# Kernel tuning notes

Hardware: AMD Instinct MI355X
Metric: run time of the kernel (lower is better)

The kernel has to match this reference:

```python
import jax, jax.numpy as jnp
import numpy as np

THETA = 10000.0
NUM_HEADS = 16


def _rope(x, positions):
    # x: [B, H, S, Dk] (fp32), positions: [B, S] int
    d_k = x.shape[-1]
    k = jnp.arange(0, d_k, 2, dtype=jnp.float32)
    freqs = THETA ** (-k / d_k)                      # [Dk/2]
    angles = positions[..., None].astype(jnp.float32) * freqs  # [B, S, Dk/2]
    cos = jnp.cos(angles)[:, None, :, :]             # [B, 1, S, Dk/2]
    sin = jnp.sin(angles)[:, None, :, :]
    xr = x.reshape(*x.shape[:-1], d_k // 2, 2)
    x_even, x_odd = xr[..., 0], xr[..., 1]
    rot_even = x_even * cos - x_odd * sin
    rot_odd = x_even * sin + x_odd * cos
    out = jnp.stack([rot_even, rot_odd], axis=-1)
    return out.reshape(x.shape)


def setup_inputs() -> dict:
    key = jax.random.key(0)
    ks = jax.random.split(key, 6)
    B, S, D = 2, 2048, 1024
    std = (2.0 / (D + D)) ** 0.5
    x = jax.random.normal(ks[0], (B, S, D), dtype=jnp.float32)
    Wq = jax.random.normal(ks[1], (D, D), dtype=jnp.float32) * std
    Wk = jax.random.normal(ks[2], (D, D), dtype=jnp.float32) * std
    Wv = jax.random.normal(ks[3], (D, D), dtype=jnp.float32) * std
    Wo = jax.random.normal(ks[4], (D, D), dtype=jnp.float32) * std
    token_positions = jnp.broadcast_to(jnp.arange(S, dtype=jnp.int32), (B, S))
    return {"x": x, "Wq": Wq, "Wk": Wk, "Wv": Wv, "Wo": Wo,
            "token_positions": token_positions}


def reference(x, Wq, Wk, Wv, Wo, token_positions):
    B, S, D = x.shape
    H = NUM_HEADS
    Dk = D // H
    # QKV projections (no bias): y = x @ W.T
    def proj(W):
        return (x @ W.T).reshape(B, S, H, Dk).transpose(0, 2, 1, 3)  # [B,H,S,Dk]
    Q, K, V = proj(Wq), proj(Wk), proj(Wv)
    Q = _rope(Q, token_positions)
    K = _rope(K, token_positions)
    scale = 1.0 / jnp.sqrt(jnp.float32(Dk))
    scores = jnp.einsum('bhqd,bhkd->bhqk', Q, K) * scale  # [B,H,S,S]
    causal = jnp.tril(jnp.ones((S, S), dtype=bool))
    scores = jnp.where(causal, scores, -jnp.inf)
    attn = jax.nn.softmax(scores.astype(jnp.float32), axis=-1)
    out = jnp.einsum('bhqk,bhkd->bhqd', attn, V)          # [B,H,S,Dk]
    out = out.transpose(0, 2, 1, 3).reshape(B, S, D)
    return out @ Wo.T
```

## Files before the change

### kernel.cpp

```cpp
#include <hip/hip_runtime.h>
#include <math.h>

#define D_MODEL 1024
#define NHEADS 16
#define DK 64
#define SEQ 2048
#define BATCH 2
#define MROWS (BATCH * SEQ)

typedef __attribute__((ext_vector_type(8))) short bfrag8;
typedef __attribute__((ext_vector_type(4))) float f32x4;
typedef unsigned short u16;
typedef __attribute__((ext_vector_type(8))) u16 u16x8;
typedef __attribute__((ext_vector_type(4))) u16 u16x4;

#define GLOBAL_AS(p) ((const __attribute__((address_space(1))) void*)(p))
#define LDS_AS(p)    ((__attribute__((address_space(3))) void*)(p))

#define RAW_BARRIER()  __asm__ volatile("s_barrier" ::: "memory")
#define WAIT_VM8()     __asm__ volatile("s_waitcnt vmcnt(8)" ::: "memory")
#define WAIT_VM4()     __asm__ volatile("s_waitcnt vmcnt(4)" ::: "memory")
#define WAIT_VM2()     __asm__ volatile("s_waitcnt vmcnt(2)" ::: "memory")
#define WAIT_VM0()     __asm__ volatile("s_waitcnt vmcnt(0)" ::: "memory")

__device__ inline u16 f2bf(float f) {
  union { float f; unsigned u; } c; c.f = f;
  unsigned r = c.u + 0x7FFF + ((c.u >> 16) & 1);
  return (u16)(r >> 16);
}

__device__ inline unsigned pack_bf2(float lo, float hi) {
  return __builtin_amdgcn_perm(__float_as_uint(hi), __float_as_uint(lo), 0x07060302);
}

struct CvtPtrs { const float* src[5]; };

__global__ __launch_bounds__(256)
void convert_and_tab(CvtPtrs p, u16* __restrict__ dst,
                     const int* __restrict__ pos, float2* __restrict__ tab) {
  const int bi = blockIdx.x;
  if (bi < 8192) {
    size_t base = ((size_t)bi * 256 + threadIdx.x) * 4;
    const size_t XSZ = (size_t)MROWS * D_MODEL;
    const float* s; size_t off;
    if (base < XSZ) { s = p.src[0]; off = base; }
    else {
      size_t j = base - XSZ;
      s = p.src[1 + (int)(j >> 20)];
      off = j & ((1u << 20) - 1);
    }
    float4 v = *(const float4*)(s + off);
    u16 o[4] = { f2bf(v.x), f2bf(v.y), f2bf(v.z), f2bf(v.w) };
    *(u16x4*)(dst + base) = *(u16x4*)o;
  } else {
    int idx = (bi - 8192) * 256 + threadIdx.x;
    int i = idx & 31, bs = idx >> 5;
    float pp = (float)pos[bs];
    float freq = expf(-(float)i * 0.2878231366242558f);
    float sn, cs;
    sincosf(pp * freq, &sn, &cs);
    tab[idx] = make_float2(cs, sn);
  }
}

__device__ inline void gemm_core(const u16* __restrict__ A, const u16* __restrict__ B,
                                 int m0, int n0, u16* As, u16* Bs,
                                 f32x4 acc[4][4]) {
  const int tid = threadIdx.x;
  const int w = tid >> 6, lane = tid & 63;
  const int l15 = lane & 15, quad = lane >> 4;
  const int wm = w >> 1, wn = w & 1;
  const int srow = tid >> 2;
  const int scol = (tid & 3) * 8;

  #pragma unroll
  for (int mi = 0; mi < 4; ++mi)
    #pragma unroll
    for (int ni = 0; ni < 4; ++ni) acc[mi][ni] = (f32x4)0.f;

  #define GSTAGE(T, BUF) do {                                                        \
    _Pragma("unroll")                                                                \
    for (int i_ = 0; i_ < 2; ++i_) {                                                 \
      const u16* ga_ = A + (size_t)((i_ * 64 + srow) + m0) * D_MODEL + (T) * 32 + scol; \
      const u16* gb_ = B + (size_t)((i_ * 64 + srow) + n0) * D_MODEL + (T) * 32 + scol; \
      __builtin_amdgcn_global_load_lds(GLOBAL_AS(ga_),                               \
          LDS_AS(&As[(BUF) * 4096 + (i_ * 64 + w * 16) * 32]), 16, 0, 0);            \
      __builtin_amdgcn_global_load_lds(GLOBAL_AS(gb_),                               \
          LDS_AS(&Bs[(BUF) * 4096 + (i_ * 64 + w * 16) * 32]), 16, 0, 0);            \
    }                                                                                \
  } while (0)

  const int NT = D_MODEL / 32;
  GSTAGE(0, 0);
  GSTAGE(1, 1);
  int sbuf = 2;
  int cbuf = 0;
  for (int t = 0; t < NT; ++t) {
    RAW_BARRIER();
    if (t + 2 < NT) {
      GSTAGE(t + 2, sbuf);
      WAIT_VM8();
    } else if (t + 1 < NT) {
      WAIT_VM4();
    } else {
      WAIT_VM0();
    }
    RAW_BARRIER();

    bfrag8 af[4], bfr[4];
    #pragma unroll
    for (int i = 0; i < 4; ++i) {
      af[i]  = *(const bfrag8*)&As[cbuf * 4096 + (wm * 64 + i * 16 + l15) * 32 + quad * 8];
      bfr[i] = *(const bfrag8*)&Bs[cbuf * 4096 + (wn * 64 + i * 16 + l15) * 32 + quad * 8];
    }
    #pragma unroll
    for (int mi = 0; mi < 4; ++mi)
      #pragma unroll
      for (int ni = 0; ni < 4; ++ni)
        acc[mi][ni] = __builtin_amdgcn_mfma_f32_16x16x32_bf16(af[mi], bfr[ni], acc[mi][ni], 0, 0, 0);

    sbuf = cbuf;
    cbuf = (cbuf == 2) ? 0 : cbuf + 1;
  }
  #undef GSTAGE
}

struct QKVArgs { const u16* A[3]; const u16* B[3]; u16* dst[3]; const float2* tab; };

__global__ __launch_bounds__(256)
void gemm_qkv_fused(QKVArgs p) {
  __shared__ u16 As[3 * 128 * 32];
  __shared__ u16 Bs[3 * 128 * 32];
  const int z = blockIdx.z;
  const int bi = blockIdx.x;
  int m0, n0;
  if (z < 2) { m0 = (bi & 7) * 128; n0 = (bi >> 3) * 128; }
  else       { m0 = (bi >> 3) * 128; n0 = (bi & 7) * 128; }
  f32x4 acc[4][4];
  gemm_core(p.A[z], p.B[z], m0, n0, As, Bs, acc);

  const int tid = threadIdx.x;
  const int w = tid >> 6, lane = tid & 63;
  const int l15 = lane & 15, quad = lane >> 4;
  const int wm = w >> 1, wn = w & 1;
  u16* dst = p.dst[z];

  if (z < 2) {
    const int head = (m0 + wm * 64) >> 6;
    const float scale = (z == 0) ? 0.125f * 1.4426950408889634f : 1.0f;
    #pragma unroll
    for (int ni = 0; ni < 4; ++ni) {
      int sg = n0 + wn * 64 + ni * 16 + l15;
      int b = sg >> 11;
      int s = sg & (SEQ - 1);
      size_t ho = ((size_t)(b * NHEADS + head)) * SEQ * DK;
      #pragma unroll
      for (int mi = 0; mi < 4; ++mi) {
        float4 t = *(const float4*)&p.tab[(size_t)sg * 32 + mi * 8 + quad * 2];
        float e0 = acc[mi][ni][0], o0 = acc[mi][ni][1];
        float e1 = acc[mi][ni][2], o1 = acc[mi][ni][3];
        u16x4 ov = { f2bf((e0 * t.x - o0 * t.y) * scale),
                     f2bf((e0 * t.y + o0 * t.x) * scale),
                     f2bf((e1 * t.z - o1 * t.w) * scale),
                     f2bf((e1 * t.w + o1 * t.z) * scale) };
        *(u16x4*)&dst[ho + (size_t)s * DK + mi * 16 + quad * 4] = ov;
      }
    }
  } else {
    const int b = m0 >> 11;
    const int head = (n0 >> 6) + wn;
    const size_t ho = ((size_t)(b * NHEADS + head)) * SEQ * DK;
    const int row_base = m0 + wm * 64;
    #pragma unroll
    for (int mi = 0; mi < 4; ++mi)
      #pragma unroll
      for (int ni = 0; ni < 4; ++ni) {
        int d = ni * 16 + l15;
        int sb = (row_base + mi * 16 + quad * 4) & (SEQ - 1);
        u16 o[4];
        #pragma unroll
        for (int r = 0; r < 4; ++r) o[r] = f2bf(acc[mi][ni][r]);
        *(u16x4*)&dst[ho + (size_t)d * SEQ + sb] = *(u16x4*)o;
      }
  }
}

__global__ __launch_bounds__(256)
void gemm_out_bf16(const u16* __restrict__ A, const u16* __restrict__ B,
                   float* __restrict__ C) {
  __shared__ u16 As[128 * 32];
  __shared__ u16 Bs[64 * 32];
  const int m0 = blockIdx.y * 128, n0 = blockIdx.x * 64;
  const int tid = threadIdx.x;
  const int w = tid >> 6, lane = tid & 63;
  const int l15 = lane & 15, quad = lane >> 4;
  const int wm = w >> 1, wn = w & 1;
  const int lrow = lane >> 2;
  const int lcol = (lane & 3) * 8;

  f32x4 acc[4][2];
  #pragma unroll
  for (int mi = 0; mi < 4; ++mi)
    #pragma unroll
    for (int ni = 0; ni < 2; ++ni) acc[mi][ni] = (f32x4)0.f;

  for (int k0 = 0; k0 < D_MODEL; k0 += 32) {
    __syncthreads();
    #pragma unroll
    for (int i = 0; i < 2; ++i) {
      int row = (i * 4 + w) * 16 + lrow;
      const u16* ga = A + (size_t)(m0 + row) * D_MODEL + k0 + lcol;
      __builtin_amdgcn_global_load_lds(GLOBAL_AS(ga), LDS_AS(&As[(i * 4 + w) * 16 * 32]), 16, 0, 0);
    }
    {
      int row = w * 16 + lrow;
      const u16* gb = B + (size_t)(n0 + row) * D_MODEL + k0 + lcol;
      __builtin_amdgcn_global_load_lds(GLOBAL_AS(gb), LDS_AS(&Bs[w * 16 * 32]), 16, 0, 0);
    }
    __syncthreads();

    bfrag8 af[4], bfr[2];
    #pragma unroll
    for (int i = 0; i < 4; ++i)
      af[i] = *(const bfrag8*)&As[(wm * 64 + i * 16 + l15) * 32 + quad * 8];
    #pragma unroll
    for (int i = 0; i < 2; ++i)
      bfr[i] = *(const bfrag8*)&Bs[(wn * 32 + i * 16 + l15) * 32 + quad * 8];
    #pragma unroll
    for (int mi = 0; mi < 4; ++mi)
      #pragma unroll
      for (int ni = 0; ni < 2; ++ni)
        acc[mi][ni] = __builtin_amdgcn_mfma_f32_16x16x32_bf16(af[mi], bfr[ni], acc[mi][ni], 0, 0, 0);
  }

  #pragma unroll
  for (int mi = 0; mi < 4; ++mi)
    #pragma unroll
    for (int ni = 0; ni < 2; ++ni)
      #pragma unroll
      for (int r = 0; r < 4; ++r) {
        int row = m0 + wm * 64 + mi * 16 + quad * 4 + r;
        int col = n0 + wn * 32 + ni * 16 + l15;
        C[(size_t)row * D_MODEL + col] = acc[mi][ni][r];
      }
}

__global__ __launch_bounds__(512, 8)
void attn_mfma(const u16* __restrict__ Qbf, const u16* __restrict__ Kbf,
               const u16* __restrict__ Vtb, u16* __restrict__ obb) {
  __shared__ u16 Ks[2][64 * 64];
  __shared__ u16 Vt[2][64 * 64];

  const int tid = threadIdx.x;
  const int w = tid >> 6, lane = tid & 63;
  const int l15 = lane & 15, quad = lane >> 4;
  const int wq = w & 3, kh = w >> 2;

  const int bid = blockIdx.x;
  const int hb = bid & 31;
  const int g  = bid >> 5;
  const int tt = (g & 7) | ((g & 16) >> 1);
  const int qt = (g & 8) ? (31 - tt) : tt;
  const int b = hb >> 4, h = hb & 15;
  const size_t ho = (size_t)hb * SEQ * DK;
  const int qrow_base = qt * 64 + wq * 16;

  bfrag8 qf[2];
  #pragma unroll
  for (int hh = 0; hh < 2; ++hh)
    qf[hh] = *(const bfrag8*)&Qbf[ho + (size_t)(qrow_base + l15) * DK + hh * 32 + quad * 8];

  f32x4 oacc[4];
  float l_ = 0.f;
  #pragma unroll
  for (int n0 = 0; n0 < 4; ++n0) oacc[n0] = (f32x4)0.f;

  const int srow = w * 8 + (lane >> 3);
  const int scc = ((lane & 7) ^ ((lane >> 3) & 7)) * 8;

  const int adr0 = (((quad & 1) << 5) + l15) << 2;
  const int adr1 = adr0 + 64;

  #define STAGE(T, BUF) do {                                                         \
    int j0_ = (T) * 64;                                                              \
    __builtin_amdgcn_global_load_lds(GLOBAL_AS(Kbf + ho + (size_t)(j0_ + srow) * DK + scc), \
                                     LDS_AS(&Ks[BUF][w * 512]), 16, 0, 0);           \
    __builtin_amdgcn_global_load_lds(GLOBAL_AS(Vtb + ho + (size_t)srow * SEQ + j0_ + scc),  \
                                     LDS_AS(&Vt[BUF][w * 512]), 16, 0, 0);           \
  } while (0)

  const int ntiles = qt + 1;
  STAGE(0, 0);

  for (int t = 0; t < ntiles; ++t) {
    const int j0 = t * 64;
    const int buf = t & 1;
    RAW_BARRIER();
    if (t + 1 < ntiles) {
      STAGE(t + 1, buf ^ 1);
      WAIT_VM2();
    } else {
      WAIT_VM0();
    }
    RAW_BARRIER();

    f32x4 sc[2];
    const int sw = l15 & 7;
    #pragma unroll
    for (int st = 0; st < 2; ++st) {
      int key = kh * 32 + st * 16 + l15;
      bfrag8 kf0 = *(const bfrag8*)&Ks[buf][key * 64 + ((quad ^ sw) * 8)];
      bfrag8 kf1 = *(const bfrag8*)&Ks[buf][key * 64 + (((4 + quad) ^ sw) * 8)];
      sc[st] = __builtin_amdgcn_mfma_f32_16x16x32_bf16(kf0, qf[0], (f32x4)0.f, 0, 0, 0);
      sc[st] = __builtin_amdgcn_mfma_f32_16x16x32_bf16(kf1, qf[1], sc[st], 0, 0, 0);
    }

    if (j0 + 63 > qrow_base) {
      #pragma unroll
      for (int st = 0; st < 2; ++st)
        #pragma unroll
        for (int r = 0; r < 4; ++r) {
          int key = j0 + kh * 32 + st * 16 + quad * 4 + r;
          if (key > qrow_base + l15) sc[st][r] = -60.f;
        }
    }

    unsigned pk[2][2];
    float rs = 0.f;
    #pragma unroll
    for (int st = 0; st < 2; ++st) {
      float p0 = __builtin_amdgcn_exp2f(fminf(sc[st][0], 60.f));
      float p1 = __builtin_amdgcn_exp2f(fminf(sc[st][1], 60.f));
      float p2 = __builtin_amdgcn_exp2f(fminf(sc[st][2], 60.f));
      float p3 = __builtin_amdgcn_exp2f(fminf(sc[st][3], 60.f));
      rs += (p0 + p1) + (p2 + p3);
      pk[st][0] = pack_bf2(p0, p1);
      pk[st][1] = pack_bf2(p2, p3);
    }
    l_ += rs;

    union PU { bfrag8 f; int i[4]; } u0;
    #pragma unroll
    for (int j = 0; j < 4; ++j) {
      const int adr = (j & 2) ? adr1 : adr0;
      int lo0 = __builtin_amdgcn_ds_bpermute(adr, (int)pk[0][j & 1]);
      int hi0 = __builtin_amdgcn_ds_bpermute(adr, (int)pk[1][j & 1]);
      u0.i[j] = (quad & 2) ? hi0 : lo0;
    }
    bfrag8 pf = u0.f;

    #pragma unroll
    for (int n0 = 0; n0 < 4; ++n0) {
      bfrag8 vf = *(const bfrag8*)&Vt[buf][(n0 * 16 + l15) * 64 + (((kh * 4 + quad) ^ sw) * 8)];
      oacc[n0] = __builtin_amdgcn_mfma_f32_16x16x32_bf16(vf, pf, oacc[n0], 0, 0, 0);
    }
  }
  #undef STAGE

  float l = l_;
  l += __shfl_xor(l, 16);
  l += __shfl_xor(l, 32);

  RAW_BARRIER();
  float* osc = (float*)Ks;
  float* lsc = (float*)Vt;
  if (kh == 1) {
    #pragma unroll
    for (int n0 = 0; n0 < 4; ++n0)
      *(f32x4*)&osc[(wq * 64 + lane) * 16 + n0 * 4] = oacc[n0];
    if (quad == 0) lsc[wq * 16 + l15] = l;
  }
  RAW_BARRIER();
  if (kh == 0) {
    float lt = l + lsc[wq * 16 + l15];
    float inv = 1.f / lt;
    int q = qrow_base + l15;
    #pragma unroll
    for (int n0 = 0; n0 < 4; ++n0) {
      f32x4 o2 = *(const f32x4*)&osc[(wq * 64 + lane) * 16 + n0 * 4];
      u16x4 ov = { f2bf((oacc[n0][0] + o2[0]) * inv), f2bf((oacc[n0][1] + o2[1]) * inv),
                   f2bf((oacc[n0][2] + o2[2]) * inv), f2bf((oacc[n0][3] + o2[3]) * inv) };
      *(u16x4*)&obb[(size_t)(b * SEQ + q) * D_MODEL + h * DK + n0 * 16 + quad * 4] = ov;
    }
  }
}

extern "C" void kernel_launch(void* const* d_in, const int* in_sizes, int n_in,
                              void* d_out, int out_size, void* d_ws, size_t ws_size,
                              hipStream_t stream) {
  const float* x  = (const float*)d_in[0];
  const float* Wq = (const float*)d_in[1];
  const float* Wk = (const float*)d_in[2];
  const float* Wv = (const float*)d_in[3];
  const float* Wo = (const float*)d_in[4];
  const int* pos  = (const int*)d_in[5];

  const size_t XSZ = (size_t)MROWS * D_MODEL;
  const size_t WSZ = (size_t)D_MODEL * D_MODEL;

  u16* bfb = (u16*)d_ws;
  u16* xb  = bfb;
  u16* wqb = xb  + XSZ;
  u16* wkb = wqb + WSZ;
  u16* wvb = wkb + WSZ;
  u16* wob = wvb + WSZ;
  u16* Qbf = wob + WSZ;
  u16* Kbf = Qbf + XSZ;
  u16* Vtb = Kbf + XSZ;
  u16* obb = Vtb + XSZ;
  float2* tab = (float2*)(obb + XSZ);

  CvtPtrs cp; cp.src[0] = x; cp.src[1] = Wq; cp.src[2] = Wk; cp.src[3] = Wv; cp.src[4] = Wo;
  convert_and_tab<<<8192 + 512, 256, 0, stream>>>(cp, xb, pos, tab);

  QKVArgs qp;
  qp.A[0] = wqb; qp.A[1] = wkb; qp.A[2] = xb;
  qp.B[0] = xb;  qp.B[1] = xb;  qp.B[2] = wvb;
  qp.dst[0] = Qbf; qp.dst[1] = Kbf; qp.dst[2] = Vtb;
  qp.tab = tab;
  gemm_qkv_fused<<<dim3(256, 1, 3), 256, 0, stream>>>(qp);

  attn_mfma<<<dim3(1024), 512, 0, stream>>>(Qbf, Kbf, Vtb, obb);

  gemm_out_bf16<<<dim3(D_MODEL / 64, MROWS / 128), 256, 0, stream>>>(obb, wob, (float*)d_out);
}
```

Baseline: 179.8 us.

## Process two adjacent query tiles per attention block to reuse staged K/V

Each attention block now handles two consecutive 64-row query tiles (2j and 2j+1), sharing every K/V tile loaded into LDS between both. This halves the grid and the K/V global-to-LDS traffic per query row, and the first tile skips work once past its causal diagonal. In exchange, register pressure roughly doubles (launch bounds lowered to 4 waves/SIMD), there are half as many blocks to balance, and the extra branches on the first tile may cause divergence.

```diff
diff --git a/kernel.cpp b/kernel.cpp
--- a/kernel.cpp
+++ b/kernel.cpp
@@ -245,11 +245,12 @@
       }
 }
 
-__global__ __launch_bounds__(512, 8)
+__global__ __launch_bounds__(512, 4)
 void attn_mfma(const u16* __restrict__ Qbf, const u16* __restrict__ Kbf,
                const u16* __restrict__ Vtb, u16* __restrict__ obb) {
   __shared__ u16 Ks[2][64 * 64];
   __shared__ u16 Vt[2][64 * 64];
+  __shared__ float lsc[2][4][16];
 
   const int tid = threadIdx.x;
   const int w = tid >> 6, lane = tid & 63;
@@ -259,21 +260,24 @@
   const int bid = blockIdx.x;
   const int hb = bid & 31;
   const int g  = bid >> 5;
-  const int tt = (g & 7) | ((g & 16) >> 1);
-  const int qt = (g & 8) ? (31 - tt) : tt;
+  const int j  = (g & 8) ? (15 - (g & 7)) : (g & 7);
+  const int qtA = 2 * j, qtB = 2 * j + 1;
   const int b = hb >> 4, h = hb & 15;
   const size_t ho = (size_t)hb * SEQ * DK;
-  const int qrow_base = qt * 64 + wq * 16;
-
-  bfrag8 qf[2];
+  const int qbA = qtA * 64 + wq * 16;
+  const int qbB = qbA + 64;
+
+  bfrag8 qfA[2], qfB[2];
   #pragma unroll
-  for (int hh = 0; hh < 2; ++hh)
-    qf[hh] = *(const bfrag8*)&Qbf[ho + (size_t)(qrow_base + l15) * DK + hh * 32 + quad * 8];
-
-  f32x4 oacc[4];
-  float l_ = 0.f;
+  for (int hh = 0; hh < 2; ++hh) {
+    qfA[hh] = *(const bfrag8*)&Qbf[ho + (size_t)(qbA + l15) * DK + hh * 32 + quad * 8];
+    qfB[hh] = *(const bfrag8*)&Qbf[ho + (size_t)(qbB + l15) * DK + hh * 32 + quad * 8];
+  }
+
+  f32x4 oA[4], oB[4];
+  float lA = 0.f, lB = 0.f;
   #pragma unroll
-  for (int n0 = 0; n0 < 4; ++n0) oacc[n0] = (f32x4)0.f;
+  for (int n0 = 0; n0 < 4; ++n0) { oA[n0] = (f32x4)0.f; oB[n0] = (f32x4)0.f; }
 
   const int srow = w * 8 + (lane >> 3);
   const int scc = ((lane & 7) ^ ((lane >> 3) & 7)) * 8;
@@ -289,7 +293,34 @@
                                      LDS_AS(&Vt[BUF][w * 512]), 16, 0, 0);           \
   } while (0)
 
-  const int ntiles = qt + 1;
+  #define SOFTMAX_PACK(SC, PK, LACC) do {                                            \
+    float rs_ = 0.f;                                                                 \
+    _Pragma("unroll")                                                                \
+    for (int st_ = 0; st_ < 2; ++st_) {                                              \
+      float p0 = __builtin_amdgcn_exp2f(fminf(SC[st_][0], 60.f));                    \
+      float p1 = __builtin_amdgcn_exp2f(fminf(SC[st_][1], 60.f));                    \
+      float p2 = __builtin_amdgcn_exp2f(fminf(SC[st_][2], 60.f));                    \
+      float p3 = __builtin_amdgcn_exp2f(fminf(SC[st_][3], 60.f));                    \
+      rs_ += (p0 + p1) + (p2 + p3);                                                  \
+      PK[st_][0] = pack_bf2(p0, p1);                                                 \
+      PK[st_][1] = pack_bf2(p2, p3);                                                 \
+    }                                                                                \
+    LACC += rs_;                                                                     \
+  } while (0)
+
+  #define PEXCH(PK, PF) do {                                                         \
+    union PU { bfrag8 f; int i[4]; } u_;                                             \
+    _Pragma("unroll")                                                                \
+    for (int j_ = 0; j_ < 4; ++j_) {                                                 \
+      const int adr_ = (j_ & 2) ? adr1 : adr0;                                       \
+      int lo_ = __builtin_amdgcn_ds_bpermute(adr_, (int)PK[0][j_ & 1]);              \
+      int hi_ = __builtin_amdgcn_ds_bpermute(adr_, (int)PK[1][j_ & 1]);              \
+      u_.i[j_] = (quad & 2) ? hi_ : lo_;                                             \
+    }                                                                                \
+    PF = u_.f;                                                                       \
+  } while (0)
+
+  const int ntiles = qtB + 1;
   STAGE(0, 0);
 
   for (int t = 0; t < ntiles; ++t) {
@@ -304,83 +335,90 @@
     }
     RAW_BARRIER();
 
-    f32x4 sc[2];
+    const bool actA = (t <= qtA);
+
+    f32x4 scA[2], scB[2];
     const int sw = l15 & 7;
     #pragma unroll
     for (int st = 0; st < 2; ++st) {
       int key = kh * 32 + st * 16 + l15;
       bfrag8 kf0 = *(const bfrag8*)&Ks[buf][key * 64 + ((quad ^ sw) * 8)];
       bfrag8 kf1 = *(const bfrag8*)&Ks[buf][key * 64 + (((4 + quad) ^ sw) * 8)];
-      sc[st] = __builtin_amdgcn_mfma_f32_16x16x32_bf16(kf0, qf[0], (f32x4)0.f, 0, 0, 0);
-      sc[st] = __builtin_amdgcn_mfma_f32_16x16x32_bf16(kf1, qf[1], sc[st], 0, 0, 0);
-    }
-
-    if (j0 + 63 > qrow_base) {
+      scB[st] = __builtin_amdgcn_mfma_f32_16x16x32_bf16(kf0, qfB[0], (f32x4)0.f, 0, 0, 0);
+      scB[st] = __builtin_amdgcn_mfma_f32_16x16x32_bf16(kf1, qfB[1], scB[st], 0, 0, 0);
+      if (actA) {
+        scA[st] = __builtin_amdgcn_mfma_f32_16x16x32_bf16(kf0, qfA[0], (f32x4)0.f, 0, 0, 0);
+        scA[st] = __builtin_amdgcn_mfma_f32_16x16x32_bf16(kf1, qfA[1], scA[st], 0, 0, 0);
+      }
+    }
+
+    if (t == qtB) {
       #pragma unroll
       for (int st = 0; st < 2; ++st)
         #pragma unroll
         for (int r = 0; r < 4; ++r) {
           int key = j0 + kh * 32 + st * 16 + quad * 4 + r;
-          if (key > qrow_base + l15) sc[st][r] = -60.f;
+          if (key > qbB + l15) scB[st][r] = -60.f;
         }
     }
-
-    unsigned pk[2][2];
-    float rs = 0.f;
-    #pragma unroll
-    for (int st = 0; st < 2; ++st) {
-      float p0 = __builtin_amdgcn_exp2f(fminf(sc[st][0], 60.f));
-      float p1 = __builtin_amdgcn_exp2f(fminf(sc[st][1], 60.f));
-      float p2 = __builtin_amdgcn_exp2f(fminf(sc[st][2], 60.f));
-      float p3 = __builtin_amdgcn_exp2f(fminf(sc[st][3], 60.f));
-      rs += (p0 + p1) + (p2 + p3);
-      pk[st][0] = pack_bf2(p0, p1);
-      pk[st][1] = pack_bf2(p2, p3);
-    }
-    l_ += rs;
-
-    union PU { bfrag8 f; int i[4]; } u0;
-    #pragma unroll
-    for (int j = 0; j < 4; ++j) {
-      const int adr = (j & 2) ? adr1 : adr0;
-      int lo0 = __builtin_amdgcn_ds_bpermute(adr, (int)pk[0][j & 1]);
-      int hi0 = __builtin_amdgcn_ds_bpermute(adr, (int)pk[1][j & 1]);
-      u0.i[j] = (quad & 2) ? hi0 : lo0;
-    }
-    bfrag8 pf = u0.f;
+    if (t == qtA) {
+      #pragma unroll
+      for (int st = 0; st < 2; ++st)
+        #pragma unroll
+        for (int r = 0; r < 4; ++r) {
+          int key = j0 + kh * 32 + st * 16 + quad * 4 + r;
+          if (key > qbA + l15) scA[st][r] = -60.f;
+        }
+    }
+
+    unsigned pkB[2][2], pkA[2][2];
+    bfrag8 pfB, pfA;
+    SOFTMAX_PACK(scB, pkB, lB);
+    PEXCH(pkB, pfB);
+    if (actA) {
+      SOFTMAX_PACK(scA, pkA, lA);
+      PEXCH(pkA, pfA);
+    }
 
     #pragma unroll
     for (int n0 = 0; n0 < 4; ++n0) {
       bfrag8 vf = *(const bfrag8*)&Vt[buf][(n0 * 16 + l15) * 64 + (((kh * 4 + quad) ^ sw) * 8)];
-      oacc[n0] = __builtin_amdgcn_mfma_f32_16x16x32_bf16(vf, pf, oacc[n0], 0, 0, 0);
+      oB[n0] = __builtin_amdgcn_mfma_f32_16x16x32_bf16(vf, pfB, oB[n0], 0, 0, 0);
+      if (actA)
+        oA[n0] = __builtin_amdgcn_mfma_f32_16x16x32_bf16(vf, pfA, oA[n0], 0, 0, 0);
     }
   }
   #undef STAGE
 
-  float l = l_;
-  l += __shfl_xor(l, 16);
-  l += __shfl_xor(l, 32);
+  lA += __shfl_xor(lA, 16); lA += __shfl_xor(lA, 32);
+  lB += __shfl_xor(lB, 16); lB += __shfl_xor(lB, 32);
 
   RAW_BARRIER();
-  float* osc = (float*)Ks;
-  float* lsc = (float*)Vt;
+  float* oscA = (float*)Ks;
+  float* oscB = (float*)Vt;
   if (kh == 1) {
     #pragma unroll
-    for (int n0 = 0; n0 < 4; ++n0)
-      *(f32x4*)&osc[(wq * 64 + lane) * 16 + n0 * 4] = oacc[n0];
-    if (quad == 0) lsc[wq * 16 + l15] = l;
+    for (int n0 = 0; n0 < 4; ++n0) {
+      *(f32x4*)&oscA[(wq * 64 + lane) * 16 + n0 * 4] = oA[n0];
+      *(f32x4*)&oscB[(wq * 64 + lane) * 16 + n0 * 4] = oB[n0];
+    }
+    if (quad == 0) { lsc[0][wq][l15] = lA; lsc[1][wq][l15] = lB; }
   }
   RAW_BARRIER();
   if (kh == 0) {
-    float lt = l + lsc[wq * 16 + l15];
-    float inv = 1.f / lt;
-    int q = qrow_base + l15;
+    float invA = 1.f / (lA + lsc[0][wq][l15]);
+    float invB = 1.f / (lB + lsc[1][wq][l15]);
+    int qA = qbA + l15, qB = qbB + l15;
     #pragma unroll
     for (int n0 = 0; n0 < 4; ++n0) {
-      f32x4 o2 = *(const f32x4*)&osc[(wq * 64 + lane) * 16 + n0 * 4];
-      u16x4 ov = { f2bf((oacc[n0][0] + o2[0]) * inv), f2bf((oacc[n0][1] + o2[1]) * inv),
-                   f2bf((oacc[n0][2] + o2[2]) * inv), f2bf((oacc[n0][3] + o2[3]) * inv) };
-      *(u16x4*)&obb[(size_t)(b * SEQ + q) * D_MODEL + h * DK + n0 * 16 + quad * 4] = ov;
+      f32x4 a2 = *(const f32x4*)&oscA[(wq * 64 + lane) * 16 + n0 * 4];
+      f32x4 b2 = *(const f32x4*)&oscB[(wq * 64 + lane) * 16 + n0 * 4];
+      u16x4 ovA = { f2bf((oA[n0][0] + a2[0]) * invA), f2bf((oA[n0][1] + a2[1]) * invA),
+                    f2bf((oA[n0][2] + a2[2]) * invA), f2bf((oA[n0][3] + a2[3]) * invA) };
+      u16x4 ovB = { f2bf((oB[n0][0] + b2[0]) * invB), f2bf((oB[n0][1] + b2[1]) * invB),
+                    f2bf((oB[n0][2] + b2[2]) * invB), f2bf((oB[n0][3] + b2[3]) * invB) };
+      *(u16x4*)&obb[(size_t)(b * SEQ + qA) * D_MODEL + h * DK + n0 * 16 + quad * 4] = ovA;
+      *(u16x4*)&obb[(size_t)(b * SEQ + qB) * D_MODEL + h * DK + n0 * 16 + quad * 4] = ovB;
     }
   }
 }
@@ -420,7 +458,7 @@
   qp.tab = tab;
   gemm_qkv_fused<<<dim3(256, 1, 3), 256, 0, stream>>>(qp);
 
-  attn_mfma<<<dim3(1024), 512, 0, stream>>>(Qbf, Kbf, Vtb, obb);
+  attn_mfma<<<dim3(512), 512, 0, stream>>>(Qbf, Kbf, Vtb, obb);
 
   gemm_out_bf16<<<dim3(D_MODEL / 64, MROWS / 128), 256, 0, stream>>>(obb, wob, (float*)d_out);
 }
```

New measurement: 184.2 us. 1.02x slower.

## Balance causal attention work by pairing query tiles and splitting KV with merge kernel

Applied to the files above, without the earlier changes.

Each attention block now pairs a short query tile with part of its mirrored long tile, so every block handles about the same number of KV tiles (~16.5). Split long tiles write unnormalized fp32 partial outputs and row sums to workspace, and a new merge kernel combines the two halves and normalizes. This targets the load imbalance of causal attention, where the old per-tile blocks ranged from 1 to 32 KV tiles. The cost is an extra kernel launch, fp32 partial traffic through global memory, and a lowered occupancy hint in launch bounds.

```diff
diff --git a/kernel.cpp b/kernel.cpp
--- a/kernel.cpp
+++ b/kernel.cpp
@@ -245,11 +245,13 @@
       }
 }
 
-__global__ __launch_bounds__(512, 8)
+__global__ __launch_bounds__(512, 4)
 void attn_mfma(const u16* __restrict__ Qbf, const u16* __restrict__ Kbf,
-               const u16* __restrict__ Vtb, u16* __restrict__ obb) {
+               const u16* __restrict__ Vtb, u16* __restrict__ obb,
+               float* __restrict__ Opart, float* __restrict__ lpart) {
   __shared__ u16 Ks[2][64 * 64];
   __shared__ u16 Vt[2][64 * 64];
+  __shared__ float lsc[4][16];
 
   const int tid = threadIdx.x;
   const int w = tid >> 6, lane = tid & 63;
@@ -258,28 +260,17 @@
 
   const int bid = blockIdx.x;
   const int hb = bid & 31;
-  const int g  = bid >> 5;
-  const int tt = (g & 7) | ((g & 16) >> 1);
-  const int qt = (g & 8) ? (31 - tt) : tt;
+  const int ii = (bid >> 5) & 15;
+  const int u  = bid >> 9;
+  const int qtA = ii, qtB = 31 - ii;
   const int b = hb >> 4, h = hb & 15;
   const size_t ho = (size_t)hb * SEQ * DK;
-  const int qrow_base = qt * 64 + wq * 16;
-
-  bfrag8 qf[2];
-  #pragma unroll
-  for (int hh = 0; hh < 2; ++hh)
-    qf[hh] = *(const bfrag8*)&Qbf[ho + (size_t)(qrow_base + l15) * DK + hh * 32 + quad * 8];
-
-  f32x4 oacc[4];
-  float l_ = 0.f;
-  #pragma unroll
-  for (int n0 = 0; n0 < 4; ++n0) oacc[n0] = (f32x4)0.f;
 
   const int srow = w * 8 + (lane >> 3);
   const int scc = ((lane & 7) ^ ((lane >> 3) & 7)) * 8;
-
   const int adr0 = (((quad & 1) << 5) + l15) << 2;
   const int adr1 = adr0 + 64;
+  const int sw = l15 & 7;
 
   #define STAGE(T, BUF) do {                                                         \
     int j0_ = (T) * 64;                                                              \
@@ -289,100 +280,173 @@
                                      LDS_AS(&Vt[BUF][w * 512]), 16, 0, 0);           \
   } while (0)
 
-  const int ntiles = qt + 1;
-  STAGE(0, 0);
-
-  for (int t = 0; t < ntiles; ++t) {
-    const int j0 = t * 64;
-    const int buf = t & 1;
-    RAW_BARRIER();
-    if (t + 1 < ntiles) {
-      STAGE(t + 1, buf ^ 1);
-      WAIT_VM2();
-    } else {
-      WAIT_VM0();
-    }
-    RAW_BARRIER();
-
-    f32x4 sc[2];
-    const int sw = l15 & 7;
-    #pragma unroll
-    for (int st = 0; st < 2; ++st) {
-      int key = kh * 32 + st * 16 + l15;
-      bfrag8 kf0 = *(const bfrag8*)&Ks[buf][key * 64 + ((quad ^ sw) * 8)];
-      bfrag8 kf1 = *(const bfrag8*)&Ks[buf][key * 64 + (((4 + quad) ^ sw) * 8)];
-      sc[st] = __builtin_amdgcn_mfma_f32_16x16x32_bf16(kf0, qf[0], (f32x4)0.f, 0, 0, 0);
-      sc[st] = __builtin_amdgcn_mfma_f32_16x16x32_bf16(kf1, qf[1], sc[st], 0, 0, 0);
-    }
-
-    if (j0 + 63 > qrow_base) {
-      #pragma unroll
-      for (int st = 0; st < 2; ++st)
+  auto run_phase = [&](int qt, int t_lo, int t_hi, f32x4* oacc, float& l_) {
+    if (t_lo >= t_hi) return;
+    const int qrow_base = qt * 64 + wq * 16;
+    bfrag8 qf[2];
+    #pragma unroll
+    for (int hh = 0; hh < 2; ++hh)
+      qf[hh] = *(const bfrag8*)&Qbf[ho + (size_t)(qrow_base + l15) * DK + hh * 32 + quad * 8];
+
+    RAW_BARRIER();
+    STAGE(t_lo, 0);
+    for (int t = t_lo; t < t_hi; ++t) {
+      const int j0 = t * 64;
+      const int buf = (t - t_lo) & 1;
+      RAW_BARRIER();
+      if (t + 1 < t_hi) {
+        STAGE(t + 1, buf ^ 1);
+        WAIT_VM2();
+      } else {
+        WAIT_VM0();
+      }
+      RAW_BARRIER();
+
+      f32x4 sc[2];
+      #pragma unroll
+      for (int st = 0; st < 2; ++st) {
+        int key = kh * 32 + st * 16 + l15;
+        bfrag8 kf0 = *(const bfrag8*)&Ks[buf][key * 64 + ((quad ^ sw) * 8)];
+        bfrag8 kf1 = *(const bfrag8*)&Ks[buf][key * 64 + (((4 + quad) ^ sw) * 8)];
+        sc[st] = __builtin_amdgcn_mfma_f32_16x16x32_bf16(kf0, qf[0], (f32x4)0.f, 0, 0, 0);
+        sc[st] = __builtin_amdgcn_mfma_f32_16x16x32_bf16(kf1, qf[1], sc[st], 0, 0, 0);
+      }
+
+      if (t == qt) {
         #pragma unroll
-        for (int r = 0; r < 4; ++r) {
-          int key = j0 + kh * 32 + st * 16 + quad * 4 + r;
-          if (key > qrow_base + l15) sc[st][r] = -60.f;
-        }
-    }
-
-    unsigned pk[2][2];
-    float rs = 0.f;
-    #pragma unroll
-    for (int st = 0; st < 2; ++st) {
-      float p0 = __builtin_amdgcn_exp2f(fminf(sc[st][0], 60.f));
-      float p1 = __builtin_amdgcn_exp2f(fminf(sc[st][1], 60.f));
-      float p2 = __builtin_amdgcn_exp2f(fminf(sc[st][2], 60.f));
-      float p3 = __builtin_amdgcn_exp2f(fminf(sc[st][3], 60.f));
-      rs += (p0 + p1) + (p2 + p3);
-      pk[st][0] = pack_bf2(p0, p1);
-      pk[st][1] = pack_bf2(p2, p3);
-    }
-    l_ += rs;
-
-    union PU { bfrag8 f; int i[4]; } u0;
-    #pragma unroll
-    for (int j = 0; j < 4; ++j) {
-      const int adr = (j & 2) ? adr1 : adr0;
-      int lo0 = __builtin_amdgcn_ds_bpermute(adr, (int)pk[0][j & 1]);
-      int hi0 = __builtin_amdgcn_ds_bpermute(adr, (int)pk[1][j & 1]);
-      u0.i[j] = (quad & 2) ? hi0 : lo0;
-    }
-    bfrag8 pf = u0.f;
-
-    #pragma unroll
-    for (int n0 = 0; n0 < 4; ++n0) {
-      bfrag8 vf = *(const bfrag8*)&Vt[buf][(n0 * 16 + l15) * 64 + (((kh * 4 + quad) ^ sw) * 8)];
-      oacc[n0] = __builtin_amdgcn_mfma_f32_16x16x32_bf16(vf, pf, oacc[n0], 0, 0, 0);
-    }
+        for (int st = 0; st < 2; ++st)
+          #pragma unroll
+          for (int r = 0; r < 4; ++r) {
+            int key = j0 + kh * 32 + st * 16 + quad * 4 + r;
+            if (key > qrow_base + l15) sc[st][r] = -60.f;
+          }
+      }
+
+      unsigned pk[2][2];
+      float rs = 0.f;
+      #pragma unroll
+      for (int st = 0; st < 2; ++st) {
+        float p0 = __builtin_amdgcn_exp2f(fminf(sc[st][0], 60.f));
+        float p1 = __builtin_amdgcn_exp2f(fminf(sc[st][1], 60.f));
+        float p2 = __builtin_amdgcn_exp2f(fminf(sc[st][2], 60.f));
+        float p3 = __builtin_amdgcn_exp2f(fminf(sc[st][3], 60.f));
+        rs += (p0 + p1) + (p2 + p3);
+        pk[st][0] = pack_bf2(p0, p1);
+        pk[st][1] = pack_bf2(p2, p3);
+      }
+      l_ += rs;
+
+      union PU { bfrag8 f; int i[4]; } u0;
+      #pragma unroll
+      for (int jj = 0; jj < 4; ++jj) {
+        const int adr = (jj & 2) ? adr1 : adr0;
+        int lo0 = __builtin_amdgcn_ds_bpermute(adr, (int)pk[0][jj & 1]);
+        int hi0 = __builtin_amdgcn_ds_bpermute(adr, (int)pk[1][jj & 1]);
+        u0.i[jj] = (quad & 2) ? hi0 : lo0;
+      }
+      bfrag8 pf = u0.f;
+
+      #pragma unroll
+      for (int n0 = 0; n0 < 4; ++n0) {
+        bfrag8 vf = *(const bfrag8*)&Vt[buf][(n0 * 16 + l15) * 64 + (((kh * 4 + quad) ^ sw) * 8)];
+        oacc[n0] = __builtin_amdgcn_mfma_f32_16x16x32_bf16(vf, pf, oacc[n0], 0, 0, 0);
+      }
+    }
+  };
+
+  auto final_store = [&](int qt, f32x4* oacc, float l_) {
+    float l = l_;
+    l += __shfl_xor(l, 16); l += __shfl_xor(l, 32);
+    RAW_BARRIER();
+    float* osc = (float*)Ks;
+    if (kh == 1) {
+      #pragma unroll
+      for (int n0 = 0; n0 < 4; ++n0)
+        *(f32x4*)&osc[(wq * 64 + lane) * 16 + n0 * 4] = oacc[n0];
+      if (quad == 0) lsc[wq][l15] = l;
+    }
+    RAW_BARRIER();
+    if (kh == 0) {
+      float inv = 1.f / (l + lsc[wq][l15]);
+      int q = qt * 64 + wq * 16 + l15;
+      #pragma unroll
+      for (int n0 = 0; n0 < 4; ++n0) {
+        f32x4 o2 = *(const f32x4*)&osc[(wq * 64 + lane) * 16 + n0 * 4];
+        u16x4 ov = { f2bf((oacc[n0][0] + o2[0]) * inv), f2bf((oacc[n0][1] + o2[1]) * inv),
+                     f2bf((oacc[n0][2] + o2[2]) * inv), f2bf((oacc[n0][3] + o2[3]) * inv) };
+        *(u16x4*)&obb[(size_t)(b * SEQ + q) * D_MODEL + h * DK + n0 * 16 + quad * 4] = ov;
+      }
+    }
+  };
+
+  auto partial_store = [&](int su, f32x4* oacc, float l_) {
+    float l = l_;
+    l += __shfl_xor(l, 16); l += __shfl_xor(l, 32);
+    RAW_BARRIER();
+    float* osc = (float*)Ks;
+    if (kh == 1) {
+      #pragma unroll
+      for (int n0 = 0; n0 < 4; ++n0)
+        *(f32x4*)&osc[(wq * 64 + lane) * 16 + n0 * 4] = oacc[n0];
+      if (quad == 0) lsc[wq][l15] = l;
+    }
+    RAW_BARRIER();
+    if (kh == 0) {
+      float lt = l + lsc[wq][l15];
+      size_t slot = (size_t)(su * 32 + hb) * 15 + ii;
+      size_t base = slot * 4096 + (size_t)(wq * 16 + l15) * 64;
+      #pragma unroll
+      for (int n0 = 0; n0 < 4; ++n0) {
+        f32x4 o2 = *(const f32x4*)&osc[(wq * 64 + lane) * 16 + n0 * 4];
+        f32x4 s = oacc[n0] + o2;
+        *(f32x4*)&Opart[base + n0 * 16 + quad * 4] = s;
+      }
+      if (quad == 0) lpart[slot * 64 + wq * 16 + l15] = lt;
+    }
+  };
+
+  f32x4 oB[4]; float lB = 0.f;
+  #pragma unroll
+  for (int n0 = 0; n0 < 4; ++n0) oB[n0] = (f32x4)0.f;
+
+  if (u == 0) {
+    f32x4 oA[4]; float lA = 0.f;
+    #pragma unroll
+    for (int n0 = 0; n0 < 4; ++n0) oA[n0] = (f32x4)0.f;
+    run_phase(qtA, 0, qtA + 1, oA, lA);
+    run_phase(qtB, 0, 15 - ii, oB, lB);
+    final_store(qtA, oA, lA);
+    if (ii < 15) partial_store(0, oB, lB);
+  } else {
+    run_phase(qtB, 15 - ii, 32 - ii, oB, lB);
+    if (ii == 15) final_store(qtB, oB, lB);
+    else partial_store(1, oB, lB);
   }
   #undef STAGE
-
-  float l = l_;
-  l += __shfl_xor(l, 16);
-  l += __shfl_xor(l, 32);
-
-  RAW_BARRIER();
-  float* osc = (float*)Ks;
-  float* lsc = (float*)Vt;
-  if (kh == 1) {
-    #pragma unroll
-    for (int n0 = 0; n0 < 4; ++n0)
-      *(f32x4*)&osc[(wq * 64 + lane) * 16 + n0 * 4] = oacc[n0];
-    if (quad == 0) lsc[wq * 16 + l15] = l;
-  }
-  RAW_BARRIER();
-  if (kh == 0) {
-    float lt = l + lsc[wq * 16 + l15];
-    float inv = 1.f / lt;
-    int q = qrow_base + l15;
-    #pragma unroll
-    for (int n0 = 0; n0 < 4; ++n0) {
-      f32x4 o2 = *(const f32x4*)&osc[(wq * 64 + lane) * 16 + n0 * 4];
-      u16x4 ov = { f2bf((oacc[n0][0] + o2[0]) * inv), f2bf((oacc[n0][1] + o2[1]) * inv),
-                   f2bf((oacc[n0][2] + o2[2]) * inv), f2bf((oacc[n0][3] + o2[3]) * inv) };
-      *(u16x4*)&obb[(size_t)(b * SEQ + q) * D_MODEL + h * DK + n0 * 16 + quad * 4] = ov;
-    }
-  }
+}
+
+__global__ __launch_bounds__(256)
+void attn_merge(const float* __restrict__ Opart, const float* __restrict__ lpart,
+                u16* __restrict__ obb) {
+  int idx = blockIdx.x * 256 + threadIdx.x;
+  int t4 = idx & 15;
+  int row = (idx >> 4) & 63;
+  int g2 = idx >> 10;
+  int pp = g2 % 15;
+  int hb = g2 / 15;
+  int qt = 31 - pp;
+  int q = qt * 64 + row;
+  int b = hb >> 4, h = hb & 15;
+  size_t s0 = ((size_t)hb * 15 + pp) * 4096 + (size_t)row * 64;
+  size_t s1 = ((size_t)(32 + hb) * 15 + pp) * 4096 + (size_t)row * 64;
+  float l = lpart[((size_t)hb * 15 + pp) * 64 + row] +
+            lpart[((size_t)(32 + hb) * 15 + pp) * 64 + row];
+  float inv = 1.f / l;
+  f32x4 a = *(const f32x4*)(Opart + s0 + t4 * 4);
+  f32x4 c = *(const f32x4*)(Opart + s1 + t4 * 4);
+  u16x4 ov = { f2bf((a[0] + c[0]) * inv), f2bf((a[1] + c[1]) * inv),
+               f2bf((a[2] + c[2]) * inv), f2bf((a[3] + c[3]) * inv) };
+  *(u16x4*)&obb[((size_t)(b * SEQ + q)) * D_MODEL + h * DK + t4 * 4] = ov;
 }
 
 extern "C" void kernel_launch(void* const* d_in, const int* in_sizes, int n_in,
@@ -409,6 +473,8 @@
   u16* Vtb = Kbf + XSZ;
   u16* obb = Vtb + XSZ;
   float2* tab = (float2*)(obb + XSZ);
+  float* Opart = (float*)(tab + 131072);
+  float* lpart = Opart + (size_t)2 * 32 * 15 * 4096;
 
   CvtPtrs cp; cp.src[0] = x; cp.src[1] = Wq; cp.src[2] = Wk; cp.src[3] = Wv; cp.src[4] = Wo;
   convert_and_tab<<<8192 + 512, 256, 0, stream>>>(cp, xb, pos, tab);
@@ -420,7 +486,9 @@
   qp.tab = tab;
   gemm_qkv_fused<<<dim3(256, 1, 3), 256, 0, stream>>>(qp);
 
-  attn_mfma<<<dim3(1024), 512, 0, stream>>>(Qbf, Kbf, Vtb, obb);
+  attn_mfma<<<dim3(1024), 512, 0, stream>>>(Qbf, Kbf, Vtb, obb, Opart, lpart);
+
+  attn_merge<<<dim3(1920), 256, 0, stream>>>(Opart, lpart, obb);
 
   gemm_out_bf16<<<dim3(D_MODEL / 64, MROWS / 128), 256, 0, stream>>>(obb, wob, (float*)d_out);
 }
```

Result: slower. 187.3 us (+4.2%).

## Triple-buffer output projection GEMM with async global-to-LDS prefetch

Applied to the files above, without the earlier changes.

The output projection GEMM now keeps three LDS stages and prefetches tiles two k-steps ahead using global_load_lds, waiting with counted vmcnt instead of draining all loads every iteration. The aim is to overlap global memory latency with the MFMA work, which the old single-buffered loop exposed in full. It triples the LDS footprint of this kernel and relies on exact vmcnt accounting, so a miscount could cause a race.

```diff
diff --git a/kernel.cpp b/kernel.cpp
--- a/kernel.cpp
+++ b/kernel.cpp
@@ -19,7 +19,9 @@
 
 #define RAW_BARRIER()  __asm__ volatile("s_barrier" ::: "memory")
 #define WAIT_VM8()     __asm__ volatile("s_waitcnt vmcnt(8)" ::: "memory")
+#define WAIT_VM6()     __asm__ volatile("s_waitcnt vmcnt(6)" ::: "memory")
 #define WAIT_VM4()     __asm__ volatile("s_waitcnt vmcnt(4)" ::: "memory")
+#define WAIT_VM3()     __asm__ volatile("s_waitcnt vmcnt(3)" ::: "memory")
 #define WAIT_VM2()     __asm__ volatile("s_waitcnt vmcnt(2)" ::: "memory")
 #define WAIT_VM0()     __asm__ volatile("s_waitcnt vmcnt(0)" ::: "memory")
 
@@ -188,8 +190,8 @@
 __global__ __launch_bounds__(256)
 void gemm_out_bf16(const u16* __restrict__ A, const u16* __restrict__ B,
                    float* __restrict__ C) {
-  __shared__ u16 As[128 * 32];
-  __shared__ u16 Bs[64 * 32];
+  __shared__ u16 As[3 * 128 * 32];
+  __shared__ u16 Bs[3 * 64 * 32];
   const int m0 = blockIdx.y * 128, n0 = blockIdx.x * 64;
   const int tid = threadIdx.x;
   const int w = tid >> 6, lane = tid & 63;
@@ -204,34 +206,55 @@
     #pragma unroll
     for (int ni = 0; ni < 2; ++ni) acc[mi][ni] = (f32x4)0.f;
 
-  for (int k0 = 0; k0 < D_MODEL; k0 += 32) {
-    __syncthreads();
-    #pragma unroll
-    for (int i = 0; i < 2; ++i) {
-      int row = (i * 4 + w) * 16 + lrow;
-      const u16* ga = A + (size_t)(m0 + row) * D_MODEL + k0 + lcol;
-      __builtin_amdgcn_global_load_lds(GLOBAL_AS(ga), LDS_AS(&As[(i * 4 + w) * 16 * 32]), 16, 0, 0);
-    }
-    {
-      int row = w * 16 + lrow;
-      const u16* gb = B + (size_t)(n0 + row) * D_MODEL + k0 + lcol;
-      __builtin_amdgcn_global_load_lds(GLOBAL_AS(gb), LDS_AS(&Bs[w * 16 * 32]), 16, 0, 0);
-    }
-    __syncthreads();
+  #define OSTAGE(T, BUF) do {                                                        \
+    _Pragma("unroll")                                                                \
+    for (int i_ = 0; i_ < 2; ++i_) {                                                 \
+      int row_ = (i_ * 4 + w) * 16 + lrow;                                           \
+      const u16* ga_ = A + (size_t)(m0 + row_) * D_MODEL + (T) * 32 + lcol;          \
+      __builtin_amdgcn_global_load_lds(GLOBAL_AS(ga_),                               \
+          LDS_AS(&As[(BUF) * 4096 + (i_ * 4 + w) * 16 * 32]), 16, 0, 0);             \
+    }                                                                                \
+    {                                                                                \
+      int row_ = w * 16 + lrow;                                                      \
+      const u16* gb_ = B + (size_t)(n0 + row_) * D_MODEL + (T) * 32 + lcol;          \
+      __builtin_amdgcn_global_load_lds(GLOBAL_AS(gb_),                               \
+          LDS_AS(&Bs[(BUF) * 2048 + w * 16 * 32]), 16, 0, 0);                        \
+    }                                                                                \
+  } while (0)
+
+  const int NT = D_MODEL / 32;
+  OSTAGE(0, 0);
+  OSTAGE(1, 1);
+  int sbuf = 2, cbuf = 0;
+  for (int t = 0; t < NT; ++t) {
+    RAW_BARRIER();
+    if (t + 2 < NT) {
+      OSTAGE(t + 2, sbuf);
+      WAIT_VM6();
+    } else if (t + 1 < NT) {
+      WAIT_VM3();
+    } else {
+      WAIT_VM0();
+    }
+    RAW_BARRIER();
 
     bfrag8 af[4], bfr[2];
     #pragma unroll
     for (int i = 0; i < 4; ++i)
-      af[i] = *(const bfrag8*)&As[(wm * 64 + i * 16 + l15) * 32 + quad * 8];
+      af[i] = *(const bfrag8*)&As[cbuf * 4096 + (wm * 64 + i * 16 + l15) * 32 + quad * 8];
     #pragma unroll
     for (int i = 0; i < 2; ++i)
-      bfr[i] = *(const bfrag8*)&Bs[(wn * 32 + i * 16 + l15) * 32 + quad * 8];
+      bfr[i] = *(const bfrag8*)&Bs[cbuf * 2048 + (wn * 32 + i * 16 + l15) * 32 + quad * 8];
     #pragma unroll
     for (int mi = 0; mi < 4; ++mi)
       #pragma unroll
       for (int ni = 0; ni < 2; ++ni)
         acc[mi][ni] = __builtin_amdgcn_mfma_f32_16x16x32_bf16(af[mi], bfr[ni], acc[mi][ni], 0, 0, 0);
-  }
+
+    sbuf = cbuf;
+    cbuf = (cbuf == 2) ? 0 : cbuf + 1;
+  }
+  #undef OSTAGE
 
   #pragma unroll
   for (int mi = 0; mi < 4; ++mi)
```

Measured after the change: 180.9 us. About the same (+0.6%).
